# Kernel tuning notes

Hardware: AMD Instinct MI355X
Metric: run time of the kernel (lower is better)

## Reference

```python
import jax, jax.numpy as jnp
import numpy as np

B, N, D = 2, 16384, 512
H = 256          # gated-attention hidden dim
C, K = 4, 8      # num classes, descriptions per class
EPS = 1e-12


def _l2norm(x):
    return x / jnp.clip(jnp.linalg.norm(x, axis=-1, keepdims=True), EPS)


def setup_inputs() -> dict:
    key = jax.random.key(0)
    ks = jax.random.split(key, 12)
    inp = {
        'x_s': jax.random.normal(ks[0], (B, N, D), jnp.float32),
        'coord_s': jax.random.uniform(ks[1], (B, N, 2), jnp.float32),
        'x_l': jax.random.normal(ks[2], (B, N, D), jnp.float32),
        'coord_l': jax.random.uniform(ks[3], (B, N, 2), jnp.float32),
        # visual_proj: Linear(D, D), stored as [in, out] (apply x @ W + b)
        'W_proj': jax.random.normal(ks[4], (D, D), jnp.float32) / np.sqrt(D),
        'b_proj': jnp.zeros((D,), jnp.float32),
        # frozen, L2-normalized text description features [C, K, D]
        'desc_feats': _l2norm(jax.random.normal(ks[5], (C, K, D), jnp.float32)),
        # GatedAttentionPooling params ([in, out] layout)
        'Wv': jax.random.normal(ks[6], (D, H), jnp.float32) / np.sqrt(D),
        'bv': jnp.zeros((H,), jnp.float32),
        'Wu': jax.random.normal(ks[7], (D, H), jnp.float32) / np.sqrt(D),
        'bu': jnp.zeros((H,), jnp.float32),
        'w_attn': jax.random.normal(ks[8], (H,), jnp.float32) / np.sqrt(H),
        'b_attn': jnp.zeros((), jnp.float32),
    }
    return inp


def _class_scores(xp, desc_feats):
    # xp: [B,N,D] normalized projected patches; desc_feats: [C,K,D]
    scale = desc_feats.shape[-1] ** (-0.5)
    sim = jnp.einsum('bnd,ckd->bnck', xp, desc_feats) * scale  # [B,N,C,K]
    attn = jax.nn.softmax(sim, axis=-1)
    # scores_c = <xp, attn @ desc_c> collapsed without materializing [B,N,C,D]
    return jnp.einsum('bnck,ckd,bnd->bnc', attn, desc_feats, xp)  # [B,N,C]


def _gated_pool(feats, Wv, bv, Wu, bu, w_attn, b_attn):
    # feats: [B,N,D]
    A_V = jnp.tanh(feats @ Wv + bv)                 # [B,N,H]
    A_U = jax.nn.sigmoid(feats @ Wu + bu)           # [B,N,H]
    A = (A_V * A_U) @ w_attn + b_attn               # [B,N]
    A = jax.nn.softmax(A, axis=1)
    return jnp.einsum('bn,bnd->bd', A, feats)       # [B,D]


def reference(x_s, coord_s, x_l, coord_l, W_proj, b_proj, desc_feats,
              Wv, bv, Wu, bu, w_attn, b_attn):
    # coords are unused by the compute path (kept for signature fidelity)
    x_s_proj = _l2norm(_l2norm(x_s) @ W_proj + b_proj)
    x_l_proj = _l2norm(_l2norm(x_l) @ W_proj + b_proj)

    class_scores_s = _class_scores(x_s_proj, desc_feats)  # [B,N,C]
    class_scores_l = _class_scores(x_l_proj, desc_feats)

    slide_s = _l2norm(_gated_pool(x_s_proj, Wv, bv, Wu, bu, w_attn, b_attn))
    slide_l = _l2norm(_gated_pool(x_l_proj, Wv, bv, Wu, bu, w_attn, b_attn))

    # text_features_low: per-class max over descriptions, L2-normalized
    text_feats = _l2norm(jnp.max(desc_feats, axis=1))      # [C,D]

    logits = slide_s @ text_feats.T + slide_l @ text_feats.T  # [B,C]
    Y_prob = jax.nn.softmax(logits, axis=1)
    Y_hat = jnp.argmax(Y_prob, axis=1)
    return Y_prob, Y_hat, class_scores_s, class_scores_l
```

## Files before the change

kernel.cpp:

```cpp
#include <hip/hip_runtime.h>
#include <math.h>

#define B_ 2
#define N_ 16384
#define D_ 512
#define C_ 4
#define K_ 8
#define ROWS (B_*N_)
#define ROWS2 (2*ROWS)
#define EPS_ 1e-12f

typedef unsigned short u16;
typedef unsigned int u32;
using short8  = __attribute__((ext_vector_type(8))) short;
using float4v = __attribute__((ext_vector_type(4))) float;

__device__ __forceinline__ u16 f2bf(float f) {
    union { float f; u32 u; } v; v.f = f;
    u32 r = v.u + 0x7fffu + ((v.u >> 16) & 1u);
    return (u16)(r >> 16);
}
__device__ __forceinline__ u32 pack2(float a, float b) {
    return (u32)f2bf(a) | ((u32)f2bf(b) << 16);
}
__device__ __forceinline__ float bf2f(u16 h) {
    union { u32 u; float f; } v; v.u = ((u32)h) << 16;
    return v.f;
}
__device__ __forceinline__ float fsigmoid(float x) { return 1.0f / (1.0f + __expf(-x)); }
__device__ __forceinline__ float ftanh(float x)    { return 1.0f - 2.0f / (__expf(2.0f * x) + 1.0f); }

__device__ __forceinline__ void load_lds16(const u16* g, u16* l) {
    __builtin_amdgcn_global_load_lds(
        (const __attribute__((address_space(1))) u32*)g,
        (__attribute__((address_space(3))) u32*)l, 16, 0, 0);
}
__device__ __forceinline__ void stage_rows8(const u16* gtile, u16* ldsTile, int g, int lane) {
    int rg = lane >> 3;
    int c  = (lane & 7) ^ rg;
    load_lds16(gtile + (size_t)(g * 8 + rg) * 512 + c * 8, ldsTile + g * 512);
}
#define AFRAG(lds, R, c) (*(const short8*)&(lds)[(R) * 64 + (((c) ^ ((R) & 7)) * 8)])
#define BFRAG(Bf, nf, ks, lane) (*(const short8*)&(Bf)[((size_t)((nf) * 16 + (ks)) << 9) + ((lane) << 3)])

__global__ __launch_bounds__(256) void prep_weights_kernel(
    const float* __restrict__ Wp, const float* __restrict__ Wv, const float* __restrict__ Wu,
    const float* __restrict__ bv, const float* __restrict__ bu, const float* __restrict__ desc,
    u16* __restrict__ WpF, u16* __restrict__ WvuF, float* __restrict__ bvu,
    u16* __restrict__ descF)
{
    int idx = blockIdx.x * 256 + threadIdx.x;
    int e = idx & 7, l = (idx >> 3) & 63, ks = (idx >> 9) & 15, nf = idx >> 13;
    int k = ks * 32 + ((l >> 4) << 3) + e;
    int n = (nf << 4) + (l & 15);
    WpF[idx] = f2bf(Wp[(size_t)k * 512 + n]);
    int half = nf & 1, h = (nf >> 1) * 16 + (l & 15);
    WvuF[idx] = f2bf(half ? Wu[(size_t)k * 256 + h] : Wv[(size_t)k * 256 + h]);
    if (idx < 512) {
        int tl = idx >> 4, pr = tl >> 1, hf = tl & 1, hh = pr * 16 + (idx & 15);
        bvu[idx] = hf ? bu[hh] : bv[hh];
    }
    if (idx < 16384) {
        int j = idx & 7, dl = (idx >> 3) & 63, g = (idx >> 9) & 1, kt = idx >> 10;
        descF[idx] = f2bf(desc[(size_t)(g * 16 + (dl & 15)) * 512 + kt * 32 + (dl >> 4) * 8 + j]);
    }
}

__global__ __launch_bounds__(256) void rownorm_cast_kernel(
    const float* __restrict__ x_s, const float* __restrict__ x_l, u16* __restrict__ xn)
{
    int wave = threadIdx.x >> 6, lane = threadIdx.x & 63;
    size_t row = (size_t)blockIdx.x * 4 + wave;
    const float* xr = (row < (size_t)ROWS) ? (x_s + row * D_)
                                           : (x_l + (row - ROWS) * D_);
    float4 a = *(const float4*)&xr[lane * 8];
    float4 b = *(const float4*)&xr[lane * 8 + 4];
    float s = a.x*a.x + a.y*a.y + a.z*a.z + a.w*a.w
            + b.x*b.x + b.y*b.y + b.z*b.z + b.w*b.w;
#pragma unroll
    for (int off = 32; off; off >>= 1) s += __shfl_xor(s, off, 64);
    float inv = 1.0f / fmaxf(sqrtf(s), EPS_);
    uint4 o;
    o.x = pack2(a.x * inv, a.y * inv);
    o.y = pack2(a.z * inv, a.w * inv);
    o.z = pack2(b.x * inv, b.y * inv);
    o.w = pack2(b.z * inv, b.w * inv);
    *(uint4*)&xn[row * D_ + lane * 8] = o;
}

__global__ __launch_bounds__(512, 2) void fused_kernel(
    const u16* __restrict__ A,
    const u16* __restrict__ BpF,
    const u16* __restrict__ BvuF,
    const u16* __restrict__ descF,
    const float* __restrict__ bias,
    const float* __restrict__ bvu, const float* __restrict__ w_attn,
    u16* __restrict__ Cp,
    float* __restrict__ invn, float* __restrict__ Araw,
    float* __restrict__ out10)
{
    __shared__ u16 ldsStage[8192];
    __shared__ u16 tile[65536];
    int t = threadIdx.x, wave = t >> 6, lane = t & 63;
    int lr = lane & 15, lq = lane >> 4;
    int wm = wave >> 2, wn = wave & 3;
    int M0 = blockIdx.x * 128;
    const u16* Arow = A + (size_t)M0 * 512;

    float4v acc1[4][8];
#pragma unroll
    for (int i = 0; i < 4; ++i)
#pragma unroll
        for (int j = 0; j < 8; ++j)
#pragma unroll
            for (int r = 0; r < 4; ++r) acc1[i][j][r] = 0.f;

#pragma unroll 1
    for (int tt = 0; tt < 8; ++tt) {
#pragma unroll
        for (int s = 0; s < 2; ++s)
            stage_rows8(Arow + tt * 64, ldsStage, wave * 2 + s, lane);
        __syncthreads();
#pragma unroll
        for (int kt = 0; kt < 2; ++kt) {
            int ks = tt * 2 + kt;
            short8 af[4], bfr[8];
#pragma unroll
            for (int i = 0; i < 4; ++i)
                af[i] = AFRAG(ldsStage, wm * 64 + i * 16 + lr, kt * 4 + lq);
#pragma unroll
            for (int j = 0; j < 8; ++j)
                bfr[j] = BFRAG(BpF, wn * 8 + j, ks, lane);
#pragma unroll
            for (int i = 0; i < 4; ++i)
#pragma unroll
                for (int j = 0; j < 8; ++j)
                    acc1[i][j] = __builtin_amdgcn_mfma_f32_16x16x32_bf16(bfr[j], af[i], acc1[i][j], 0, 0, 0);
        }
        __syncthreads();
    }

    {
        float4 b4[8];
#pragma unroll
        for (int j = 0; j < 8; ++j)
            b4[j] = *(const float4*)&bias[wn * 128 + j * 16 + lq * 4];
#pragma unroll
        for (int i = 0; i < 4; ++i) {
            int row = wm * 64 + i * 16 + lr;
            u16* crow = Cp + (size_t)(M0 + row) * 512;
#pragma unroll
            for (int j = 0; j < 8; ++j) {
                int col = wn * 128 + j * 16 + lq * 4;
                u16 h0 = f2bf(acc1[i][j][0] + b4[j].x);
                u16 h1 = f2bf(acc1[i][j][1] + b4[j].y);
                u16 h2 = f2bf(acc1[i][j][2] + b4[j].z);
                u16 h3 = f2bf(acc1[i][j][3] + b4[j].w);
                uint2 o;
                o.x = (u32)h0 | ((u32)h1 << 16);
                o.y = (u32)h2 | ((u32)h3 << 16);
                *(uint2*)&crow[col] = o;
                int kc = col >> 6, cc = col & 63;
                int c8 = cc >> 3, off8 = cc & 7;
                *(uint2*)&tile[kc * 8192 + row * 64 + ((c8 ^ (row & 7)) * 8) + off8] = o;
            }
        }
    }
    __syncthreads();

    float4v acc2[4][8];
    float4v accS[2], accG;
#pragma unroll
    for (int i = 0; i < 4; ++i)
#pragma unroll
        for (int j = 0; j < 8; ++j)
#pragma unroll
            for (int r = 0; r < 4; ++r) acc2[i][j][r] = 0.f;
#pragma unroll
    for (int r = 0; r < 4; ++r) { accS[0][r] = 0.f; accS[1][r] = 0.f; accG[r] = 0.f; }

#pragma unroll 1
    for (int tt = 0; tt < 8; ++tt) {
        const u16* tch = tile + tt * 8192;
#pragma unroll
        for (int kt = 0; kt < 2; ++kt) {
            int ks = tt * 2 + kt;
            short8 afc = AFRAG(tch, wave * 16 + lr, kt * 4 + lq);
            short8 d0 = *(const short8*)&descF[((ks * 2 + 0) << 9) + (lane << 3)];
            short8 d1 = *(const short8*)&descF[((ks * 2 + 1) << 9) + (lane << 3)];
            accS[0] = __builtin_amdgcn_mfma_f32_16x16x32_bf16(afc, d0, accS[0], 0, 0, 0);
            accS[1] = __builtin_amdgcn_mfma_f32_16x16x32_bf16(afc, d1, accS[1], 0, 0, 0);
            accG    = __builtin_amdgcn_mfma_f32_16x16x32_bf16(afc, afc, accG, 0, 0, 0);
            short8 af[4], bfr[8];
#pragma unroll
            for (int i = 0; i < 4; ++i)
                af[i] = AFRAG(tch, wm * 64 + i * 16 + lr, kt * 4 + lq);
#pragma unroll
            for (int j = 0; j < 8; ++j)
                bfr[j] = BFRAG(BvuF, wn * 8 + j, ks, lane);
#pragma unroll
            for (int i = 0; i < 4; ++i)
#pragma unroll
                for (int j = 0; j < 8; ++j)
                    acc2[i][j] = __builtin_amdgcn_mfma_f32_16x16x32_bf16(bfr[j], af[i], acc2[i][j], 0, 0, 0);
        }
    }

    float* sInvF = (float*)ldsStage;
    float* redA  = ((float*)ldsStage) + 128;
#pragma unroll
    for (int r = 0; r < 4; ++r) {
        if (lr == lq * 4 + r) {
            float iv = 1.0f / fmaxf(sqrtf(accG[r]), EPS_);
            sInvF[wave * 16 + lq * 4 + r] = iv;
            invn[M0 + wave * 16 + lq * 4 + r] = iv;
        }
    }
    __syncthreads();

    {
        const float scale = 0.04419417382415922f;
        int side = (M0 >= ROWS) ? 1 : 0;
        float* cls = out10 + (size_t)side * ((size_t)ROWS * 4);
        int rbase = M0 - side * ROWS + wave * 16;
#pragma unroll
        for (int r = 0; r < 4; ++r) {
            int rloc = rbase + lq * 4 + r;
            float iv = sInvF[wave * 16 + lq * 4 + r];
            float sv0 = accS[0][r] * iv, sv1 = accS[1][r] * iv;
#pragma unroll
            for (int g = 0; g < 2; ++g) {
                float s = g ? sv1 : sv0;
                float ts = s * scale;
                float mx = ts;
                mx = fmaxf(mx, __shfl_xor(mx, 1, 64));
                mx = fmaxf(mx, __shfl_xor(mx, 2, 64));
                mx = fmaxf(mx, __shfl_xor(mx, 4, 64));
                float e = __expf(ts - mx);
                float num = e * s, den = e;
                num += __shfl_xor(num, 1, 64); den += __shfl_xor(den, 1, 64);
                num += __shfl_xor(num, 2, 64); den += __shfl_xor(den, 2, 64);
                num += __shfl_xor(num, 4, 64); den += __shfl_xor(den, 4, 64);
                if ((lr & 7) == 0) {
                    int c = g * 2 + ((lr >> 3) & 1);
                    cls[(size_t)rloc * 4 + c] = num / den;
                }
            }
        }
    }

    {
        int colbase = wn * 128;
        int hbase = wn * 64;
        float4 bv4[4], bu4[4], w4[4];
#pragma unroll
        for (int p = 0; p < 4; ++p) {
            int nv = colbase + p * 32 + lq * 4;
            bv4[p] = *(const float4*)&bvu[nv];
            bu4[p] = *(const float4*)&bvu[nv + 16];
            w4[p]  = *(const float4*)&w_attn[hbase + p * 16 + lq * 4];
        }
#pragma unroll
        for (int i = 0; i < 4; ++i) {
            int rloc = wm * 64 + i * 16 + lr;
            float iv = sInvF[rloc];
            float part = 0.f;
#pragma unroll
            for (int p = 0; p < 4; ++p) {
#pragma unroll
                for (int r = 0; r < 4; ++r) {
                    float v = acc2[i][2 * p][r] * iv + (&bv4[p].x)[r];
                    float u = acc2[i][2 * p + 1][r] * iv + (&bu4[p].x)[r];
                    part += ftanh(v) * (&w4[p].x)[r] * fsigmoid(u);
                }
            }
            part += __shfl_xor(part, 16, 64);
            part += __shfl_xor(part, 32, 64);
            if (lq == 0) redA[wn * 128 + rloc] = part;
        }
    }
    __syncthreads();
    if (t < 128)
        Araw[M0 + t] = redA[t] + redA[128 + t] + redA[256 + t] + redA[384 + t];
}

__global__ __launch_bounds__(256) void areduce_kernel(
    const float* __restrict__ Araw, float* __restrict__ part)
{
    __shared__ float red[256];
    int t = threadIdx.x, g = blockIdx.y;
    size_t i0 = (size_t)g * N_ + blockIdx.x * 512 + t * 2;
    float2 v = *(const float2*)&Araw[i0];
    red[t] = fmaxf(v.x, v.y); __syncthreads();
    for (int s = 128; s; s >>= 1) { if (t < s) red[t] = fmaxf(red[t], red[t + s]); __syncthreads(); }
    float m = red[0]; __syncthreads();
    red[t] = __expf(v.x - m) + __expf(v.y - m); __syncthreads();
    for (int s = 128; s; s >>= 1) { if (t < s) red[t] += red[t + s]; __syncthreads(); }
    if (t == 0) {
        int pi = g * 32 + blockIdx.x;
        part[pi * 2] = m;
        part[pi * 2 + 1] = red[0];
    }
}

__global__ __launch_bounds__(128) void acombine_kernel(
    const float* __restrict__ part, float* __restrict__ mg)
{
    int t = threadIdx.x;
    int g = t >> 5, j = t & 31;
    float m = part[(g * 32 + j) * 2];
    float s = part[(g * 32 + j) * 2 + 1];
    float mm = m;
#pragma unroll
    for (int off = 1; off < 32; off <<= 1) mm = fmaxf(mm, __shfl_xor(mm, off, 64));
    float sc = s * __expf(m - mm);
#pragma unroll
    for (int off = 1; off < 32; off <<= 1) sc += __shfl_xor(sc, off, 64);
    if (j == 0) {
        mg[g * 2] = mm;
        mg[g * 2 + 1] = 1.0f / sc;
    }
}

__global__ __launch_bounds__(256) void pool_kernel(
    const float* __restrict__ Araw, const float* __restrict__ invn,
    const float* __restrict__ mg, const u16* __restrict__ xpraw,
    float* __restrict__ slideAll)
{
    __shared__ float lds[4][512];
    int t = threadIdx.x, wave = t >> 6, lane = t & 63;
    int g = blockIdx.y;
    float m = mg[g * 2], is = mg[g * 2 + 1];
    size_t row0 = (size_t)g * N_ + (size_t)blockIdx.x * 256 + wave;
    float a[8] = {};
    for (int r = 0; r < 64; ++r) {
        size_t row = row0 + r * 4;
        float av = __expf(Araw[row] - m) * is * invn[row];
        uint4 pk = *(const uint4*)&xpraw[row * D_ + lane * 8];
        a[0] += av * bf2f((u16)pk.x); a[1] += av * bf2f((u16)(pk.x >> 16));
        a[2] += av * bf2f((u16)pk.y); a[3] += av * bf2f((u16)(pk.y >> 16));
        a[4] += av * bf2f((u16)pk.z); a[5] += av * bf2f((u16)(pk.z >> 16));
        a[6] += av * bf2f((u16)pk.w); a[7] += av * bf2f((u16)(pk.w >> 16));
    }
#pragma unroll
    for (int i = 0; i < 8; ++i) lds[wave][lane * 8 + i] = a[i];
    __syncthreads();
#pragma unroll
    for (int q = 0; q < 2; ++q) {
        int c = t * 2 + q;
        float s = lds[0][c] + lds[1][c] + lds[2][c] + lds[3][c];
        atomicAdd(&slideAll[(size_t)g * 512 + c], s);
    }
}

__global__ __launch_bounds__(512) void finalize_kernel(
    const float* __restrict__ slide_s, const float* __restrict__ slide_l,
    const float* __restrict__ desc, float* __restrict__ out)
{
    __shared__ float txt[4][512];
    __shared__ float ssn[2][512];
    __shared__ float sln[2][512];
    __shared__ float red[512];
    __shared__ float lg[8];
    int t = threadIdx.x;

    auto reduceSum = [&](float v) -> float {
        red[t] = v; __syncthreads();
        for (int s = 256; s; s >>= 1) { if (t < s) red[t] += red[t + s]; __syncthreads(); }
        float r = red[0]; __syncthreads();
        return r;
    };

    for (int c = 0; c < 4; ++c) {
        float m = -1e30f;
        for (int k = 0; k < 8; ++k) m = fmaxf(m, desc[((size_t)c * 8 + k) * 512 + t]);
        float ss = reduceSum(m * m);
        txt[c][t] = m / fmaxf(sqrtf(ss), EPS_);
    }
    for (int b = 0; b < 2; ++b) {
        float v = slide_s[b * 512 + t];
        float ss = reduceSum(v * v);
        ssn[b][t] = v / fmaxf(sqrtf(ss), EPS_);
        v = slide_l[b * 512 + t];
        ss = reduceSum(v * v);
        sln[b][t] = v / fmaxf(sqrtf(ss), EPS_);
    }
    __syncthreads();
    for (int b = 0; b < 2; ++b)
        for (int c = 0; c < 4; ++c) {
            float v = ssn[b][t] * txt[c][t] + sln[b][t] * txt[c][t];
            float s = reduceSum(v);
            if (t == 0) lg[b * 4 + c] = s;
        }
    __syncthreads();
    if (t < 2) {
        int b = t;
        float m = -1e30f;
        for (int c = 0; c < 4; ++c) m = fmaxf(m, lg[b * 4 + c]);
        float e[4]; float den = 0.f;
        for (int c = 0; c < 4; ++c) { e[c] = expf(lg[b * 4 + c] - m); den += e[c]; }
        int am = 0; float bm = -1.f;
        for (int c = 0; c < 4; ++c) {
            float pcl = e[c] / den;
            out[b * 4 + c] = pcl;
            if (pcl > bm) { bm = pcl; am = c; }
        }
        out[8 + b] = (float)am;
    }
}

extern "C" void kernel_launch(void* const* d_in, const int* in_sizes, int n_in,
                              void* d_out, int out_size, void* d_ws, size_t ws_size,
                              hipStream_t stream) {
    const float* x_s    = (const float*)d_in[0];
    const float* x_l    = (const float*)d_in[2];
    const float* W_proj = (const float*)d_in[4];
    const float* b_proj = (const float*)d_in[5];
    const float* desc   = (const float*)d_in[6];
    const float* Wv     = (const float*)d_in[7];
    const float* bv     = (const float*)d_in[8];
    const float* Wu     = (const float*)d_in[9];
    const float* bu     = (const float*)d_in[10];
    const float* w_attn = (const float*)d_in[11];
    float* out = (float*)d_out;

    char* w = (char*)d_ws;
    u16* xn        = (u16*)w;
    u16* xpraw     = (u16*)(w + 67108864);
    u16* WpF       = (u16*)(w + 134217728);
    u16* WvuF      = (u16*)(w + 134742016);
    u16* descF     = (u16*)(w + 135266304);
    float* bvu     = (float*)(w + 135299072);
    float* invn    = (float*)(w + 135301120);
    float* Araw    = (float*)(w + 135563264);
    float* part    = (float*)(w + 135825408);
    float* mg      = (float*)(w + 135826432);
    float* slideAll= (float*)(w + 135827456);

    hipMemsetAsync(slideAll, 0, 8192, stream);
    prep_weights_kernel<<<1024, 256, 0, stream>>>(W_proj, Wv, Wu, bv, bu, desc,
                                                  WpF, WvuF, bvu, descF);

    rownorm_cast_kernel<<<ROWS2 / 4, 256, 0, stream>>>(x_s, x_l, xn);
    fused_kernel<<<512, 512, 0, stream>>>(xn, WpF, WvuF, descF, b_proj, bvu, w_attn,
                                          xpraw, invn, Araw, out + 10);
    areduce_kernel<<<dim3(32, 4), 256, 0, stream>>>(Araw, part);
    acombine_kernel<<<1, 128, 0, stream>>>(part, mg);
    pool_kernel<<<dim3(64, 4), 256, 0, stream>>>(Araw, invn, mg, xpraw, slideAll);
    finalize_kernel<<<1, 512, 0, stream>>>(slideAll, slideAll + 1024, desc, out);
}
```

Measured before the change: 322.4 us.

## Pipeline A staging through the tile buffer and merge softmax reduction kernels

```diff
diff --git a/kernel.cpp b/kernel.cpp
--- a/kernel.cpp
+++ b/kernel.cpp
@@ -99,8 +99,9 @@
     float* __restrict__ invn, float* __restrict__ Araw,
     float* __restrict__ out10)
 {
-    __shared__ u16 ldsStage[8192];
     __shared__ u16 tile[65536];
+    __shared__ float sInvF[128];
+    __shared__ float redA[512];
     int t = threadIdx.x, wave = t >> 6, lane = t & 63;
     int lr = lane & 15, lq = lane >> 4;
     int wm = wave >> 2, wn = wave & 3;
@@ -115,30 +116,58 @@
 #pragma unroll
             for (int r = 0; r < 4; ++r) acc1[i][j][r] = 0.f;
 
+#define STAGE1(c) { stage_rows8(Arow + (c) * 64, tile + (size_t)(c) * 8192, wave * 2 + 0, lane); \
+                    stage_rows8(Arow + (c) * 64, tile + (size_t)(c) * 8192, wave * 2 + 1, lane); }
+#define GCOMP1(TCH, BR) \
+    { _Pragma("unroll") \
+      for (int kt = 0; kt < 2; ++kt) { \
+          short8 af[4]; \
+          _Pragma("unroll") \
+          for (int i_ = 0; i_ < 4; ++i_) \
+              af[i_] = AFRAG(TCH, wm * 64 + i_ * 16 + lr, kt * 4 + lq); \
+          _Pragma("unroll") \
+          for (int i_ = 0; i_ < 4; ++i_) \
+              _Pragma("unroll") \
+              for (int j_ = 0; j_ < 8; ++j_) \
+                  acc1[i_][j_] = __builtin_amdgcn_mfma_f32_16x16x32_bf16(BR[kt * 8 + j_], af[i_], acc1[i_][j_], 0, 0, 0); \
+      } }
+#define LOADB1(BR, ttv) \
+    { _Pragma("unroll") \
+      for (int j_ = 0; j_ < 8; ++j_) { \
+          BR[j_]     = BFRAG(BpF, wn * 8 + j_, (ttv) * 2 + 0, lane); \
+          BR[8 + j_] = BFRAG(BpF, wn * 8 + j_, (ttv) * 2 + 1, lane); \
+      } }
+
+    STAGE1(0); STAGE1(1);
+    asm volatile("s_waitcnt vmcnt(2)" ::: "memory");
+    __builtin_amdgcn_s_barrier();
+
 #pragma unroll 1
-    for (int tt = 0; tt < 8; ++tt) {
-#pragma unroll
-        for (int s = 0; s < 2; ++s)
-            stage_rows8(Arow + tt * 64, ldsStage, wave * 2 + s, lane);
-        __syncthreads();
-#pragma unroll
-        for (int kt = 0; kt < 2; ++kt) {
-            int ks = tt * 2 + kt;
-            short8 af[4], bfr[8];
-#pragma unroll
-            for (int i = 0; i < 4; ++i)
-                af[i] = AFRAG(ldsStage, wm * 64 + i * 16 + lr, kt * 4 + lq);
-#pragma unroll
-            for (int j = 0; j < 8; ++j)
-                bfr[j] = BFRAG(BpF, wn * 8 + j, ks, lane);
-#pragma unroll
-            for (int i = 0; i < 4; ++i)
-#pragma unroll
-                for (int j = 0; j < 8; ++j)
-                    acc1[i][j] = __builtin_amdgcn_mfma_f32_16x16x32_bf16(bfr[j], af[i], acc1[i][j], 0, 0, 0);
-        }
-        __syncthreads();
-    }
+    for (int tt = 0; tt < 6; ++tt) {
+        short8 bfr[16];
+        LOADB1(bfr, tt);
+        asm volatile("" ::: "memory");
+        STAGE1(tt + 2);
+        const u16* tch = tile + (size_t)tt * 8192;
+        GCOMP1(tch, bfr);
+        asm volatile("s_waitcnt vmcnt(2)" ::: "memory");
+        __builtin_amdgcn_s_barrier();
+    }
+    {
+        short8 bfr[16];
+        LOADB1(bfr, 6);
+        const u16* tch = tile + (size_t)6 * 8192;
+        GCOMP1(tch, bfr);
+        asm volatile("s_waitcnt vmcnt(0)" ::: "memory");
+        __builtin_amdgcn_s_barrier();
+    }
+    {
+        short8 bfr[16];
+        LOADB1(bfr, 7);
+        const u16* tch = tile + (size_t)7 * 8192;
+        GCOMP1(tch, bfr);
+    }
+    __syncthreads();
 
     {
         float4 b4[8];
@@ -179,9 +208,9 @@
 #pragma unroll
     for (int r = 0; r < 4; ++r) { accS[0][r] = 0.f; accS[1][r] = 0.f; accG[r] = 0.f; }
 
-#pragma unroll 1
+#pragma unroll 2
     for (int tt = 0; tt < 8; ++tt) {
-        const u16* tch = tile + tt * 8192;
+        const u16* tch = tile + (size_t)tt * 8192;
 #pragma unroll
         for (int kt = 0; kt < 2; ++kt) {
             int ks = tt * 2 + kt;
@@ -206,8 +235,6 @@
         }
     }
 
-    float* sInvF = (float*)ldsStage;
-    float* redA  = ((float*)ldsStage) + 128;
 #pragma unroll
     for (int r = 0; r < 4; ++r) {
         if (lr == lq * 4 + r) {
@@ -284,41 +311,30 @@
         Araw[M0 + t] = redA[t] + redA[128 + t] + redA[256 + t] + redA[384 + t];
 }
 
-__global__ __launch_bounds__(256) void areduce_kernel(
-    const float* __restrict__ Araw, float* __restrict__ part)
+__global__ __launch_bounds__(256) void asoftmax_kernel(
+    const float* __restrict__ Araw, float* __restrict__ mg)
 {
     __shared__ float red[256];
-    int t = threadIdx.x, g = blockIdx.y;
-    size_t i0 = (size_t)g * N_ + blockIdx.x * 512 + t * 2;
-    float2 v = *(const float2*)&Araw[i0];
-    red[t] = fmaxf(v.x, v.y); __syncthreads();
+    int t = threadIdx.x, g = blockIdx.x;
+    const float4* a4 = (const float4*)(Araw + (size_t)g * N_);
+    float m = -1e30f;
+    for (int i = t; i < N_ / 4; i += 256) {
+        float4 v = a4[i];
+        m = fmaxf(m, fmaxf(fmaxf(v.x, v.y), fmaxf(v.z, v.w)));
+    }
+    red[t] = m; __syncthreads();
     for (int s = 128; s; s >>= 1) { if (t < s) red[t] = fmaxf(red[t], red[t + s]); __syncthreads(); }
-    float m = red[0]; __syncthreads();
-    red[t] = __expf(v.x - m) + __expf(v.y - m); __syncthreads();
+    m = red[0]; __syncthreads();
+    float e = 0.f;
+    for (int i = t; i < N_ / 4; i += 256) {
+        float4 v = a4[i];
+        e += __expf(v.x - m) + __expf(v.y - m) + __expf(v.z - m) + __expf(v.w - m);
+    }
+    red[t] = e; __syncthreads();
     for (int s = 128; s; s >>= 1) { if (t < s) red[t] += red[t + s]; __syncthreads(); }
     if (t == 0) {
-        int pi = g * 32 + blockIdx.x;
-        part[pi * 2] = m;
-        part[pi * 2 + 1] = red[0];
-    }
-}
-
-__global__ __launch_bounds__(128) void acombine_kernel(
-    const float* __restrict__ part, float* __restrict__ mg)
-{
-    int t = threadIdx.x;
-    int g = t >> 5, j = t & 31;
-    float m = part[(g * 32 + j) * 2];
-    float s = part[(g * 32 + j) * 2 + 1];
-    float mm = m;
-#pragma unroll
-    for (int off = 1; off < 32; off <<= 1) mm = fmaxf(mm, __shfl_xor(mm, off, 64));
-    float sc = s * __expf(m - mm);
-#pragma unroll
-    for (int off = 1; off < 32; off <<= 1) sc += __shfl_xor(sc, off, 64);
-    if (j == 0) {
-        mg[g * 2] = mm;
-        mg[g * 2 + 1] = 1.0f / sc;
+        mg[g * 2] = m;
+        mg[g * 2 + 1] = 1.0f / red[0];
     }
 }
 
@@ -433,9 +449,8 @@
     float* bvu     = (float*)(w + 135299072);
     float* invn    = (float*)(w + 135301120);
     float* Araw    = (float*)(w + 135563264);
-    float* part    = (float*)(w + 135825408);
-    float* mg      = (float*)(w + 135826432);
-    float* slideAll= (float*)(w + 135827456);
+    float* mg      = (float*)(w + 135825408);
+    float* slideAll= (float*)(w + 135826432);
 
     hipMemsetAsync(slideAll, 0, 8192, stream);
     prep_weights_kernel<<<1024, 256, 0, stream>>>(W_proj, Wv, Wu, bv, bu, desc,
@@ -444,8 +459,7 @@
     rownorm_cast_kernel<<<ROWS2 / 4, 256, 0, stream>>>(x_s, x_l, xn);
     fused_kernel<<<512, 512, 0, stream>>>(xn, WpF, WvuF, descF, b_proj, bvu, w_attn,
                                           xpraw, invn, Araw, out + 10);
-    areduce_kernel<<<dim3(32, 4), 256, 0, stream>>>(Araw, part);
-    acombine_kernel<<<1, 128, 0, stream>>>(part, mg);
+    asoftmax_kernel<<<4, 256, 0, stream>>>(Araw, mg);
     pool_kernel<<<dim3(64, 4), 256, 0, stream>>>(Araw, invn, mg, xpraw, slideAll);
     finalize_kernel<<<1, 512, 0, stream>>>(slideAll, slideAll + 1024, desc, out);
 }
```

Result: slower. 385.4 us (+19.6%).

## Merge prep/rownorm kernels and fold softmax stats and finalize via last-block counters

Applied to the files above, without the earlier changes.

```diff
diff --git a/kernel.cpp b/kernel.cpp
--- a/kernel.cpp
+++ b/kernel.cpp
@@ -43,49 +43,55 @@
 #define AFRAG(lds, R, c) (*(const short8*)&(lds)[(R) * 64 + (((c) ^ ((R) & 7)) * 8)])
 #define BFRAG(Bf, nf, ks, lane) (*(const short8*)&(Bf)[((size_t)((nf) * 16 + (ks)) << 9) + ((lane) << 3)])
 
-__global__ __launch_bounds__(256) void prep_weights_kernel(
+__global__ __launch_bounds__(256) void pre_kernel(
+    const float* __restrict__ x_s, const float* __restrict__ x_l, u16* __restrict__ xn,
     const float* __restrict__ Wp, const float* __restrict__ Wv, const float* __restrict__ Wu,
     const float* __restrict__ bv, const float* __restrict__ bu, const float* __restrict__ desc,
     u16* __restrict__ WpF, u16* __restrict__ WvuF, float* __restrict__ bvu,
-    u16* __restrict__ descF)
+    u16* __restrict__ descF, float* __restrict__ slideAll, u32* __restrict__ cnts)
 {
-    int idx = blockIdx.x * 256 + threadIdx.x;
-    int e = idx & 7, l = (idx >> 3) & 63, ks = (idx >> 9) & 15, nf = idx >> 13;
-    int k = ks * 32 + ((l >> 4) << 3) + e;
-    int n = (nf << 4) + (l & 15);
-    WpF[idx] = f2bf(Wp[(size_t)k * 512 + n]);
-    int half = nf & 1, h = (nf >> 1) * 16 + (l & 15);
-    WvuF[idx] = f2bf(half ? Wu[(size_t)k * 256 + h] : Wv[(size_t)k * 256 + h]);
-    if (idx < 512) {
-        int tl = idx >> 4, pr = tl >> 1, hf = tl & 1, hh = pr * 16 + (idx & 15);
-        bvu[idx] = hf ? bu[hh] : bv[hh];
-    }
-    if (idx < 16384) {
-        int j = idx & 7, dl = (idx >> 3) & 63, g = (idx >> 9) & 1, kt = idx >> 10;
-        descF[idx] = f2bf(desc[(size_t)(g * 16 + (dl & 15)) * 512 + kt * 32 + (dl >> 4) * 8 + j]);
-    }
-}
-
-__global__ __launch_bounds__(256) void rownorm_cast_kernel(
-    const float* __restrict__ x_s, const float* __restrict__ x_l, u16* __restrict__ xn)
-{
-    int wave = threadIdx.x >> 6, lane = threadIdx.x & 63;
-    size_t row = (size_t)blockIdx.x * 4 + wave;
-    const float* xr = (row < (size_t)ROWS) ? (x_s + row * D_)
-                                           : (x_l + (row - ROWS) * D_);
-    float4 a = *(const float4*)&xr[lane * 8];
-    float4 b = *(const float4*)&xr[lane * 8 + 4];
-    float s = a.x*a.x + a.y*a.y + a.z*a.z + a.w*a.w
-            + b.x*b.x + b.y*b.y + b.z*b.z + b.w*b.w;
-#pragma unroll
-    for (int off = 32; off; off >>= 1) s += __shfl_xor(s, off, 64);
-    float inv = 1.0f / fmaxf(sqrtf(s), EPS_);
-    uint4 o;
-    o.x = pack2(a.x * inv, a.y * inv);
-    o.y = pack2(a.z * inv, a.w * inv);
-    o.z = pack2(b.x * inv, b.y * inv);
-    o.w = pack2(b.z * inv, b.w * inv);
-    *(uint4*)&xn[row * D_ + lane * 8] = o;
+    int bid = blockIdx.x;
+    if (bid < 16384) {
+        int wave = threadIdx.x >> 6, lane = threadIdx.x & 63;
+        size_t row = (size_t)bid * 4 + wave;
+        const float* xr = (row < (size_t)ROWS) ? (x_s + row * D_)
+                                               : (x_l + (row - ROWS) * D_);
+        float4 a = *(const float4*)&xr[lane * 8];
+        float4 b = *(const float4*)&xr[lane * 8 + 4];
+        float s = a.x*a.x + a.y*a.y + a.z*a.z + a.w*a.w
+                + b.x*b.x + b.y*b.y + b.z*b.z + b.w*b.w;
+#pragma unroll
+        for (int off = 32; off; off >>= 1) s += __shfl_xor(s, off, 64);
+        float inv = 1.0f / fmaxf(sqrtf(s), EPS_);
+        uint4 o;
+        o.x = pack2(a.x * inv, a.y * inv);
+        o.y = pack2(a.z * inv, a.w * inv);
+        o.z = pack2(b.x * inv, b.y * inv);
+        o.w = pack2(b.z * inv, b.w * inv);
+        *(uint4*)&xn[row * D_ + lane * 8] = o;
+    } else {
+        int pb = bid - 16384;
+        int idx = pb * 256 + threadIdx.x;
+        int e = idx & 7, l = (idx >> 3) & 63, ks = (idx >> 9) & 15, nf = idx >> 13;
+        int k = ks * 32 + ((l >> 4) << 3) + e;
+        int n = (nf << 4) + (l & 15);
+        WpF[idx] = f2bf(Wp[(size_t)k * 512 + n]);
+        int half = nf & 1, h = (nf >> 1) * 16 + (l & 15);
+        WvuF[idx] = f2bf(half ? Wu[(size_t)k * 256 + h] : Wv[(size_t)k * 256 + h]);
+        if (idx < 512) {
+            int tl = idx >> 4, pr = tl >> 1, hf = tl & 1, hh = pr * 16 + (idx & 15);
+            bvu[idx] = hf ? bu[hh] : bv[hh];
+        }
+        if (idx < 16384) {
+            int j = idx & 7, dl = (idx >> 3) & 63, g = (idx >> 9) & 1, kt = idx >> 10;
+            descF[idx] = f2bf(desc[(size_t)(g * 16 + (dl & 15)) * 512 + kt * 32 + (dl >> 4) * 8 + j]);
+        }
+        if (pb == 0) {
+            int t = threadIdx.x;
+            for (int i = t; i < 2048; i += 256) slideAll[i] = 0.f;
+            if (t < 2) cnts[t] = 0u;
+        }
+    }
 }
 
 __global__ __launch_bounds__(512, 2) void fused_kernel(
@@ -97,10 +103,13 @@
     const float* __restrict__ bvu, const float* __restrict__ w_attn,
     u16* __restrict__ Cp,
     float* __restrict__ invn, float* __restrict__ Araw,
-    float* __restrict__ out10)
+    float* __restrict__ out10, float* __restrict__ mg, u32* __restrict__ cnt)
 {
     __shared__ u16 ldsStage[8192];
     __shared__ u16 tile[65536];
+    __shared__ float sInvF[128];
+    __shared__ float redA[512];
+    __shared__ int isLastS;
     int t = threadIdx.x, wave = t >> 6, lane = t & 63;
     int lr = lane & 15, lq = lane >> 4;
     int wm = wave >> 2, wn = wave & 3;
@@ -179,9 +188,9 @@
 #pragma unroll
     for (int r = 0; r < 4; ++r) { accS[0][r] = 0.f; accS[1][r] = 0.f; accG[r] = 0.f; }
 
-#pragma unroll 1
+#pragma unroll 2
     for (int tt = 0; tt < 8; ++tt) {
-        const u16* tch = tile + tt * 8192;
+        const u16* tch = tile + (size_t)tt * 8192;
 #pragma unroll
         for (int kt = 0; kt < 2; ++kt) {
             int ks = tt * 2 + kt;
@@ -206,8 +215,6 @@
         }
     }
 
-    float* sInvF = (float*)ldsStage;
-    float* redA  = ((float*)ldsStage) + 128;
 #pragma unroll
     for (int r = 0; r < 4; ++r) {
         if (lr == lq * 4 + r) {
@@ -282,59 +289,50 @@
     __syncthreads();
     if (t < 128)
         Araw[M0 + t] = redA[t] + redA[128 + t] + redA[256 + t] + redA[384 + t];
-}
-
-__global__ __launch_bounds__(256) void areduce_kernel(
-    const float* __restrict__ Araw, float* __restrict__ part)
-{
-    __shared__ float red[256];
-    int t = threadIdx.x, g = blockIdx.y;
-    size_t i0 = (size_t)g * N_ + blockIdx.x * 512 + t * 2;
-    float2 v = *(const float2*)&Araw[i0];
-    red[t] = fmaxf(v.x, v.y); __syncthreads();
-    for (int s = 128; s; s >>= 1) { if (t < s) red[t] = fmaxf(red[t], red[t + s]); __syncthreads(); }
-    float m = red[0]; __syncthreads();
-    red[t] = __expf(v.x - m) + __expf(v.y - m); __syncthreads();
-    for (int s = 128; s; s >>= 1) { if (t < s) red[t] += red[t + s]; __syncthreads(); }
-    if (t == 0) {
-        int pi = g * 32 + blockIdx.x;
-        part[pi * 2] = m;
-        part[pi * 2 + 1] = red[0];
-    }
-}
-
-__global__ __launch_bounds__(128) void acombine_kernel(
-    const float* __restrict__ part, float* __restrict__ mg)
-{
-    int t = threadIdx.x;
-    int g = t >> 5, j = t & 31;
-    float m = part[(g * 32 + j) * 2];
-    float s = part[(g * 32 + j) * 2 + 1];
-    float mm = m;
-#pragma unroll
-    for (int off = 1; off < 32; off <<= 1) mm = fmaxf(mm, __shfl_xor(mm, off, 64));
-    float sc = s * __expf(m - mm);
-#pragma unroll
-    for (int off = 1; off < 32; off <<= 1) sc += __shfl_xor(sc, off, 64);
-    if (j == 0) {
-        mg[g * 2] = mm;
-        mg[g * 2 + 1] = 1.0f / sc;
-    }
-}
-
-__global__ __launch_bounds__(256) void pool_kernel(
+
+    __threadfence();
+    __syncthreads();
+    if (t == 0) isLastS = (atomicAdd(cnt, 1u) == 511u) ? 1 : 0;
+    __syncthreads();
+    if (isLastS) {
+        __threadfence();
+        for (int g = 0; g < 4; ++g) {
+            const float* ag = Araw + (size_t)g * N_;
+            float m = -1e30f;
+            for (int i = t; i < N_; i += 512) m = fmaxf(m, ag[i]);
+            redA[t] = m; __syncthreads();
+            for (int s = 256; s; s >>= 1) { if (t < s) redA[t] = fmaxf(redA[t], redA[t + s]); __syncthreads(); }
+            m = redA[0]; __syncthreads();
+            float e = 0.f;
+            for (int i = t; i < N_; i += 512) e += __expf(ag[i] - m);
+            redA[t] = e; __syncthreads();
+            for (int s = 256; s; s >>= 1) { if (t < s) redA[t] += redA[t + s]; __syncthreads(); }
+            if (t == 0) { mg[g * 2] = m; mg[g * 2 + 1] = 1.0f / redA[0]; }
+            __syncthreads();
+        }
+    }
+}
+
+__global__ __launch_bounds__(512) void pool_kernel(
     const float* __restrict__ Araw, const float* __restrict__ invn,
     const float* __restrict__ mg, const u16* __restrict__ xpraw,
-    float* __restrict__ slideAll)
+    float* __restrict__ slideAll,
+    const float* __restrict__ desc, float* __restrict__ out, u32* __restrict__ cnt)
 {
-    __shared__ float lds[4][512];
+    __shared__ float lds[8][512];
+    __shared__ float txt[4][512];
+    __shared__ float ssn[2][512];
+    __shared__ float sln[2][512];
+    __shared__ float red[512];
+    __shared__ float lg[8];
+    __shared__ int lastS;
     int t = threadIdx.x, wave = t >> 6, lane = t & 63;
     int g = blockIdx.y;
     float m = mg[g * 2], is = mg[g * 2 + 1];
     size_t row0 = (size_t)g * N_ + (size_t)blockIdx.x * 256 + wave;
     float a[8] = {};
-    for (int r = 0; r < 64; ++r) {
-        size_t row = row0 + r * 4;
+    for (int r = 0; r < 32; ++r) {
+        size_t row = row0 + r * 8;
         float av = __expf(Araw[row] - m) * is * invn[row];
         uint4 pk = *(const uint4*)&xpraw[row * D_ + lane * 8];
         a[0] += av * bf2f((u16)pk.x); a[1] += av * bf2f((u16)(pk.x >> 16));
@@ -345,67 +343,66 @@
 #pragma unroll
     for (int i = 0; i < 8; ++i) lds[wave][lane * 8 + i] = a[i];
     __syncthreads();
-#pragma unroll
-    for (int q = 0; q < 2; ++q) {
-        int c = t * 2 + q;
-        float s = lds[0][c] + lds[1][c] + lds[2][c] + lds[3][c];
+    {
+        int c = t;
+        float s = lds[0][c] + lds[1][c] + lds[2][c] + lds[3][c]
+                + lds[4][c] + lds[5][c] + lds[6][c] + lds[7][c];
         atomicAdd(&slideAll[(size_t)g * 512 + c], s);
     }
-}
-
-__global__ __launch_bounds__(512) void finalize_kernel(
-    const float* __restrict__ slide_s, const float* __restrict__ slide_l,
-    const float* __restrict__ desc, float* __restrict__ out)
-{
-    __shared__ float txt[4][512];
-    __shared__ float ssn[2][512];
-    __shared__ float sln[2][512];
-    __shared__ float red[512];
-    __shared__ float lg[8];
-    int t = threadIdx.x;
-
-    auto reduceSum = [&](float v) -> float {
-        red[t] = v; __syncthreads();
-        for (int s = 256; s; s >>= 1) { if (t < s) red[t] += red[t + s]; __syncthreads(); }
-        float r = red[0]; __syncthreads();
-        return r;
-    };
-
-    for (int c = 0; c < 4; ++c) {
-        float m = -1e30f;
-        for (int k = 0; k < 8; ++k) m = fmaxf(m, desc[((size_t)c * 8 + k) * 512 + t]);
-        float ss = reduceSum(m * m);
-        txt[c][t] = m / fmaxf(sqrtf(ss), EPS_);
-    }
-    for (int b = 0; b < 2; ++b) {
-        float v = slide_s[b * 512 + t];
-        float ss = reduceSum(v * v);
-        ssn[b][t] = v / fmaxf(sqrtf(ss), EPS_);
-        v = slide_l[b * 512 + t];
-        ss = reduceSum(v * v);
-        sln[b][t] = v / fmaxf(sqrtf(ss), EPS_);
-    }
-    __syncthreads();
-    for (int b = 0; b < 2; ++b)
+
+    __threadfence();
+    __syncthreads();
+    if (t == 0) lastS = (atomicAdd(cnt, 1u) == 255u) ? 1 : 0;
+    __syncthreads();
+    if (!lastS) return;
+    __threadfence();
+    {
+        const float* slide_s = slideAll;
+        const float* slide_l = slideAll + 1024;
+
+        auto reduceSum = [&](float v) -> float {
+            red[t] = v; __syncthreads();
+            for (int s = 256; s; s >>= 1) { if (t < s) red[t] += red[t + s]; __syncthreads(); }
+            float r = red[0]; __syncthreads();
+            return r;
+        };
+
         for (int c = 0; c < 4; ++c) {
-            float v = ssn[b][t] * txt[c][t] + sln[b][t] * txt[c][t];
-            float s = reduceSum(v);
-            if (t == 0) lg[b * 4 + c] = s;
-        }
-    __syncthreads();
-    if (t < 2) {
-        int b = t;
-        float m = -1e30f;
-        for (int c = 0; c < 4; ++c) m = fmaxf(m, lg[b * 4 + c]);
-        float e[4]; float den = 0.f;
-        for (int c = 0; c < 4; ++c) { e[c] = expf(lg[b * 4 + c] - m); den += e[c]; }
-        int am = 0; float bm = -1.f;
-        for (int c = 0; c < 4; ++c) {
-            float pcl = e[c] / den;
-            out[b * 4 + c] = pcl;
-            if (pcl > bm) { bm = pcl; am = c; }
-        }
-        out[8 + b] = (float)am;
+            float mm = -1e30f;
+            for (int k = 0; k < 8; ++k) mm = fmaxf(mm, desc[((size_t)c * 8 + k) * 512 + t]);
+            float ss = reduceSum(mm * mm);
+            txt[c][t] = mm / fmaxf(sqrtf(ss), EPS_);
+        }
+        for (int b = 0; b < 2; ++b) {
+            float v = slide_s[b * 512 + t];
+            float ss = reduceSum(v * v);
+            ssn[b][t] = v / fmaxf(sqrtf(ss), EPS_);
+            v = slide_l[b * 512 + t];
+            ss = reduceSum(v * v);
+            sln[b][t] = v / fmaxf(sqrtf(ss), EPS_);
+        }
+        __syncthreads();
+        for (int b = 0; b < 2; ++b)
+            for (int c = 0; c < 4; ++c) {
+                float v = ssn[b][t] * txt[c][t] + sln[b][t] * txt[c][t];
+                float s = reduceSum(v);
+                if (t == 0) lg[b * 4 + c] = s;
+            }
+        __syncthreads();
+        if (t < 2) {
+            int b = t;
+            float mm = -1e30f;
+            for (int c = 0; c < 4; ++c) mm = fmaxf(mm, lg[b * 4 + c]);
+            float e[4]; float den = 0.f;
+            for (int c = 0; c < 4; ++c) { e[c] = expf(lg[b * 4 + c] - mm); den += e[c]; }
+            int am = 0; float bm = -1.f;
+            for (int c = 0; c < 4; ++c) {
+                float pcl = e[c] / den;
+                out[b * 4 + c] = pcl;
+                if (pcl > bm) { bm = pcl; am = c; }
+            }
+            out[8 + b] = (float)am;
+        }
     }
 }
 
@@ -433,19 +430,15 @@
     float* bvu     = (float*)(w + 135299072);
     float* invn    = (float*)(w + 135301120);
     float* Araw    = (float*)(w + 135563264);
-    float* part    = (float*)(w + 135825408);
-    float* mg      = (float*)(w + 135826432);
-    float* slideAll= (float*)(w + 135827456);
-
-    hipMemsetAsync(slideAll, 0, 8192, stream);
-    prep_weights_kernel<<<1024, 256, 0, stream>>>(W_proj, Wv, Wu, bv, bu, desc,
-                                                  WpF, WvuF, bvu, descF);
-
-    rownorm_cast_kernel<<<ROWS2 / 4, 256, 0, stream>>>(x_s, x_l, xn);
+    float* mg      = (float*)(w + 135825408);
+    float* slideAll= (float*)(w + 135826432);
+    u32* cnts      = (u32*)(w + 135834624);
+
+    pre_kernel<<<17408, 256, 0, stream>>>(x_s, x_l, xn,
+                                          W_proj, Wv, Wu, bv, bu, desc,
+                                          WpF, WvuF, bvu, descF, slideAll, cnts);
     fused_kernel<<<512, 512, 0, stream>>>(xn, WpF, WvuF, descF, b_proj, bvu, w_attn,
-                                          xpraw, invn, Araw, out + 10);
-    areduce_kernel<<<dim3(32, 4), 256, 0, stream>>>(Araw, part);
-    acombine_kernel<<<1, 128, 0, stream>>>(part, mg);
-    pool_kernel<<<dim3(64, 4), 256, 0, stream>>>(Araw, invn, mg, xpraw, slideAll);
-    finalize_kernel<<<1, 512, 0, stream>>>(slideAll, slideAll + 1024, desc, out);
-}
+                                          xpraw, invn, Araw, out + 10, mg, cnts);
+    pool_kernel<<<dim3(64, 4), 512, 0, stream>>>(Araw, invn, mg, xpraw, slideAll,
+                                                 desc, out, cnts + 1);
+}
```

Result: slower. 504.5 us (+56.5%).
